# Optimization experiments

Measured on AMD Instinct MI355X. Metric: run time of the kernel, lower is better.

The kernel has to match this reference:

```python
import jax, jax.numpy as jnp
import numpy as np

N = 100000      # total nodes in batched SEAL subgraphs
E = 1600000     # total edges
B = 512         # number of subgraphs (batch of graphs)
F = 128         # input feature dim (data.x + DRNL one-hot, pre-concatenated)
H = 128         # gnn_hidden_channels
L = 3           # num_hops == num GNN hidden layers
K = 100         # sort-pool k
D_TOT = H * L + 1              # 385, total_latent_dim
C1, C2, KW2 = 16, 32, 5        # conv1d channels / kernel
DENSE = ((K - 2) // 2 + 1 - KW2 + 1) * C2   # 1472
MLP_H = 128


def setup_inputs() -> dict:
    key = jax.random.key(0)
    ks = jax.random.split(key, 20)
    s = 0.05
    inp = {
        "x": jax.random.normal(ks[0], (N, F), jnp.float32),
        "edge_index": jax.random.randint(ks[1], (2, E), 0, N, dtype=jnp.int32).astype(jnp.int64),
        "batch": jnp.sort(jax.random.randint(ks[2], (N,), 0, B, dtype=jnp.int32)).astype(jnp.int64),
        "k": K,
        # GCN layer weights: F->H, H->H, H->H, H->1
        "Wg0": jax.random.normal(ks[3], (F, H), jnp.float32) * s, "bg0": jnp.zeros((H,), jnp.float32),
        "Wg1": jax.random.normal(ks[4], (H, H), jnp.float32) * s, "bg1": jnp.zeros((H,), jnp.float32),
        "Wg2": jax.random.normal(ks[5], (H, H), jnp.float32) * s, "bg2": jnp.zeros((H,), jnp.float32),
        "Wg3": jax.random.normal(ks[6], (H, 1), jnp.float32) * s, "bg3": jnp.zeros((1,), jnp.float32),
        # Conv1d(1, 16, kernel=D_TOT, stride=D_TOT): equivalent to per-node dense [16, D_TOT]
        "W1": jax.random.normal(ks[7], (C1, D_TOT), jnp.float32) * s, "b1": jnp.zeros((C1,), jnp.float32),
        # Conv1d(16, 32, 5, 1)
        "W2": jax.random.normal(ks[8], (C2, C1, KW2), jnp.float32) * s, "b2": jnp.zeros((C2,), jnp.float32),
        # MLP [dense, mlp_hidden, 1]
        "Wm1": jax.random.normal(ks[9], (DENSE, MLP_H), jnp.float32) * s, "bm1": jnp.zeros((MLP_H,), jnp.float32),
        "Wm2": jax.random.normal(ks[10], (MLP_H, 1), jnp.float32) * s, "bm2": jnp.zeros((1,), jnp.float32),
    }
    return inp


def reference(x, edge_index, batch, k,
              Wg0, bg0, Wg1, bg1, Wg2, bg2, Wg3, bg3,
              W1, b1, W2, b2, Wm1, bm1, Wm2, bm2):
    n = x.shape[0]
    src, dst = edge_index[0], edge_index[1]
    loop = jnp.arange(n)
    srcL = jnp.concatenate([src, loop])   # add self-loops (GCNConv default)
    dstL = jnp.concatenate([dst, loop])
    deg = jax.ops.segment_sum(jnp.ones(srcL.shape[0], x.dtype), dstL, num_segments=n)
    dinv = jnp.where(deg > 0, jax.lax.rsqrt(deg), 0.0)
    norm = (dinv[srcL] * dinv[dstL])[:, None]   # symmetric normalization

    def gcn(h, W, b):
        msg = (h @ W)[srcL] * norm                      # [E+N, out]
        return jax.ops.segment_sum(msg, dstL, num_segments=n) + b

    xs = []
    h = x
    for W, b in ((Wg0, bg0), (Wg1, bg1), (Wg2, bg2), (Wg3, bg3)):
        h = jnp.tanh(gcn(h, W, b))
        xs.append(h)
    feat = jnp.concatenate(xs, axis=-1)                 # [n, D_TOT]

    # --- SortAggregation(k): per-graph sort by last channel, descending ---
    counts = jax.ops.segment_sum(jnp.ones(n, jnp.int32), batch, num_segments=B)
    # tanh output in [-1,1], so batch*4 dominates; ascending sort => grouped by graph,
    # descending within each graph by last channel.
    sort_key = batch.astype(feat.dtype) * 4.0 - feat[:, -1]
    feat_s = feat[jnp.argsort(sort_key)]
    starts = jnp.cumsum(counts) - counts                # exclusive prefix sum
    idx = starts[:, None] + jnp.arange(k)[None, :]      # [B, k]
    valid = jnp.arange(k)[None, :] < counts[:, None]
    pooled = jnp.where(valid[:, :, None], feat_s[jnp.clip(idx, 0, n - 1)], 0.0)  # [B, k, D_TOT]

    # conv1: Conv1d(1, 16, kernel=D_TOT, stride=D_TOT) on [B,1,k*D_TOT]
    h1 = jax.nn.relu(jnp.einsum('bkd,od->bok', pooled, W1) + b1[None, :, None])  # [B,16,k]
    # maxpool1d(2,2)
    h1 = h1.reshape(h1.shape[0], h1.shape[1], -1, 2).max(axis=-1)                # [B,16,k//2]
    # conv2: Conv1d(16, 32, 5, 1)
    h2 = jax.lax.conv_general_dilated(h1, W2, window_strides=(1,), padding='VALID',
                                      dimension_numbers=('NCH', 'OIH', 'NCH'))
    h2 = jax.nn.relu(h2 + b2[None, :, None])                                     # [B,32,k//2-4]
    flat = h2.reshape(h2.shape[0], -1)                                           # [B, DENSE]
    # MLP (dropout inactive at inference)
    hid = jax.nn.relu(flat @ Wm1 + bm1)
    return hid @ Wm2 + bm2                                                       # [B, 1]
```

## Files before the change

kernel.cpp:

```cpp
#include <hip/hip_runtime.h>
#include <hip/hip_bf16.h>
#include <cfloat>

#define F_IN   128
#define H_DIM  128
#define D_TOT  385
#define KTOP   100
#define C1     16
#define C2     32
#define KW2    5
#define POOLW  (KTOP/2)
#define CONV2W (POOLW - KW2 + 1)
#define DENSE  (C2*CONV2W)
#define MLPH   128
#define SORT_CAP 2048
#define D_PAD  388
#define C1SLOTS 32
#define SCHUNK 1024
#define AGG_NPB 8

__global__ void hist_kernel(const int* __restrict__ keys, int n, int nbins, int* __restrict__ cnt) {
    int i = blockIdx.x * blockDim.x + threadIdx.x;
    if (i < n) {
        int k = keys[i];
        k = (k < 0) ? 0 : (k >= nbins ? nbins - 1 : k);
        atomicAdd(&cnt[k], 1);
    }
}

__global__ void scan_excl_kernel(const int* __restrict__ cnt, int n,
                                 int* __restrict__ start, int* __restrict__ cursor,
                                 float* __restrict__ dinv) {
    __shared__ int s[1024];
    __shared__ int carry_s;
    int tid = threadIdx.x;
    if (tid == 0) carry_s = 0;
    __syncthreads();
    for (int base = 0; base < n; base += 1024) {
        int i = base + tid;
        int v = (i < n) ? cnt[i] : 0;
        s[tid] = v;
        __syncthreads();
        for (int off = 1; off < 1024; off <<= 1) {
            int t = (tid >= off) ? s[tid - off] : 0;
            __syncthreads();
            s[tid] += t;
            __syncthreads();
        }
        int excl = s[tid] - v;
        int carry = carry_s;
        if (i < n) {
            start[i] = carry + excl;
            if (cursor) cursor[i] = carry + excl;
            if (dinv)   dinv[i]   = rsqrtf((float)v + 1.0f);
        }
        __syncthreads();
        if (tid == 0) carry_s += s[1023];
        __syncthreads();
    }
}

__global__ __launch_bounds__(256) void chunksum_kernel(const int* __restrict__ cnt, int n,
                                                       int* __restrict__ bsum) {
    __shared__ int red[256];
    int blk = blockIdx.x, tid = threadIdx.x;
    int base = blk * SCHUNK;
    int s = 0;
    for (int idx = tid; idx < SCHUNK; idx += 256) {
        int i = base + idx;
        s += (i < n) ? cnt[i] : 0;
    }
    red[tid] = s; __syncthreads();
    for (int off = 128; off > 0; off >>= 1) {
        if (tid < off) red[tid] += red[tid + off];
        __syncthreads();
    }
    if (tid == 0) bsum[blk] = red[0];
}

__global__ __launch_bounds__(256) void scan_apply_kernel(const int* __restrict__ cnt, int n,
                                                         const int* __restrict__ bstart,
                                                         int* __restrict__ start,
                                                         int* __restrict__ cursor,
                                                         float* __restrict__ dinv) {
    __shared__ int tsum[256];
    int blk = blockIdx.x, tid = threadIdx.x;
    int base = blk * SCHUNK + tid * 4;
    int v[4];
    #pragma unroll
    for (int k = 0; k < 4; k++) { int i = base + k; v[k] = (i < n) ? cnt[i] : 0; }
    int loc = v[0] + v[1] + v[2] + v[3];
    tsum[tid] = loc; __syncthreads();
    int x = loc;
    for (int off = 1; off < 256; off <<= 1) {
        int t = (tid >= off) ? tsum[tid - off] : 0;
        __syncthreads();
        x += t; tsum[tid] = x;
        __syncthreads();
    }
    int run = x - loc + bstart[blk];
    #pragma unroll
    for (int k = 0; k < 4; k++) {
        int i = base + k;
        if (i < n) {
            start[i]  = run;
            cursor[i] = run;
            dinv[i]   = rsqrtf((float)v[k] + 1.0f);
        }
        run += v[k];
    }
}

__global__ void csr_fill_kernel(const int* __restrict__ src, const int* __restrict__ dst, int e, int n,
                                int* __restrict__ cursor, const float* __restrict__ dinv,
                                int* __restrict__ csr_src, float* __restrict__ csr_w) {
    int i = blockIdx.x * blockDim.x + threadIdx.x;
    if (i < e) {
        int s = src[i], d = dst[i];
        s = (s < 0) ? 0 : (s >= n ? n - 1 : s);
        d = (d < 0) ? 0 : (d >= n ? n - 1 : d);
        int pos = atomicAdd(&cursor[d], 1);
        csr_src[pos] = s;
        csr_w[pos]   = dinv[s] * dinv[d];
    }
}

__global__ __launch_bounds__(256) void gemm_nk128(const float* __restrict__ A, int lda,
                                                  const float* __restrict__ W,
                                                  float* __restrict__ T, int n) {
    __shared__ float Al[64 * 128];
    __shared__ float Wl[128 * 64];
    int tid = threadIdx.x;
    int brow = blockIdx.x * 64;
    int chalf = blockIdx.y;

    for (int kk = tid >> 4; kk < 128; kk += 16) {
        int c4 = tid & 15;
        float4 w = *(const float4*)&W[kk * 128 + chalf * 64 + c4 * 4];
        *(float4*)&Wl[kk * 64 + c4 * 4] = w;
    }
    for (int idx = tid; idx < 64 * 128; idx += 256) {
        int rr = idx >> 7, k = idx & 127;
        int r = brow + rr;
        float a = (r < n) ? A[(size_t)r * lda + k] : 0.0f;
        Al[rr * 128 + (k ^ (rr & 31))] = a;
    }
    __syncthreads();

    int tr = tid >> 4, tc = tid & 15;
    int r0 = tr * 4;
    float acc[4][4] = {};
    #pragma unroll 4
    for (int k = 0; k < 128; k++) {
        float4 w = *(const float4*)&Wl[k * 64 + tc * 4];
        float a0 = Al[(r0 + 0) * 128 + (k ^ ((r0 + 0) & 31))];
        float a1 = Al[(r0 + 1) * 128 + (k ^ ((r0 + 1) & 31))];
        float a2 = Al[(r0 + 2) * 128 + (k ^ ((r0 + 2) & 31))];
        float a3 = Al[(r0 + 3) * 128 + (k ^ ((r0 + 3) & 31))];
        acc[0][0] += a0 * w.x; acc[0][1] += a0 * w.y; acc[0][2] += a0 * w.z; acc[0][3] += a0 * w.w;
        acc[1][0] += a1 * w.x; acc[1][1] += a1 * w.y; acc[1][2] += a1 * w.z; acc[1][3] += a1 * w.w;
        acc[2][0] += a2 * w.x; acc[2][1] += a2 * w.y; acc[2][2] += a2 * w.z; acc[2][3] += a2 * w.w;
        acc[3][0] += a3 * w.x; acc[3][1] += a3 * w.y; acc[3][2] += a3 * w.z; acc[3][3] += a3 * w.w;
    }
    for (int i = 0; i < 4; i++) {
        int r = brow + r0 + i;
        if (r < n) {
            float4 o = make_float4(acc[i][0], acc[i][1], acc[i][2], acc[i][3]);
            *(float4*)&T[(size_t)r * 128 + chalf * 64 + tc * 4] = o;
        }
    }
}

__global__ __launch_bounds__(256) void gcn_agg128(const float* __restrict__ T,
                                                  const int* __restrict__ csr_src,
                                                  const float* __restrict__ csr_w,
                                                  const int* __restrict__ row_start,
                                                  const int* __restrict__ cnt,
                                                  const float* __restrict__ dinv,
                                                  const float* __restrict__ bias,
                                                  float* __restrict__ feat, int layer, int n,
                                                  const float* __restrict__ Wg3,
                                                  float* __restrict__ T3) {
    int g    = threadIdx.x >> 5;
    int lane = threadIdx.x & 31;
    int i = blockIdx.x * AGG_NPB + g;
    if (i >= n) return;
    int c4 = lane << 2;
    float di = dinv[i];
    float s2 = di * di;
    float4 self = *(const float4*)&T[(size_t)i * 128 + c4];
    float4 acc = make_float4(self.x * s2, self.y * s2, self.z * s2, self.w * s2);
    int rs = row_start[i], ce = cnt[i];
    for (int e = 0; e < ce; e++) {
        int s  = csr_src[rs + e];
        float w = csr_w[rs + e];
        float4 v = *(const float4*)&T[(size_t)s * 128 + c4];
        acc.x += v.x * w; acc.y += v.y * w; acc.z += v.z * w; acc.w += v.w * w;
    }
    float4 bb = *(const float4*)&bias[c4];
    float4 vt = make_float4(tanhf(acc.x + bb.x), tanhf(acc.y + bb.y),
                            tanhf(acc.z + bb.z), tanhf(acc.w + bb.w));
    float* fout = &feat[(size_t)i * D_TOT + layer * 128 + c4];
    fout[0] = vt.x; fout[1] = vt.y; fout[2] = vt.z; fout[3] = vt.w;
    if (T3 != nullptr) {
        float4 wg = *(const float4*)&Wg3[c4];
        float4 p = make_float4(vt.x * wg.x, vt.y * wg.y, vt.z * wg.z, vt.w * wg.w);
        #pragma unroll
        for (int off = 16; off > 0; off >>= 1) {
            p.x += __shfl_down(p.x, off, 32);
            p.y += __shfl_down(p.y, off, 32);
            p.z += __shfl_down(p.z, off, 32);
            p.w += __shfl_down(p.w, off, 32);
        }
        if (lane == 0) T3[i] = (p.x + p.z) + (p.y + p.w);
    }
}

__global__ void gcn_agg1(const float* __restrict__ T3,
                         const int* __restrict__ csr_src, const float* __restrict__ csr_w,
                         const int* __restrict__ row_start, const int* __restrict__ cnt,
                         const float* __restrict__ dinv, const float* __restrict__ bg3,
                         float* __restrict__ feat, int n) {
    int i = blockIdx.x * blockDim.x + threadIdx.x;
    if (i >= n) return;
    float di = dinv[i];
    float acc = T3[i] * di * di;
    int rs = row_start[i], ce = cnt[i];
    for (int e = 0; e < ce; e++) acc += T3[csr_src[rs + e]] * csr_w[rs + e];
    feat[(size_t)i * D_TOT + (D_TOT - 1)] = tanhf(acc + bg3[0]);
}

__global__ __launch_bounds__(256) void sortpool_kernel(const float* __restrict__ feat,
                                                       const int* __restrict__ gcnt,
                                                       const int* __restrict__ gstart,
                                                       int* __restrict__ sel) {
    int b = blockIdx.x, tid = threadIdx.x;
    __shared__ float sv[SORT_CAP];
    __shared__ int   si[SORT_CAP];
    int cnt = gcnt[b];
    if (cnt > SORT_CAP) cnt = SORT_CAP;
    int start = gstart[b];
    if (cnt == 0) {
        for (int j = tid; j < KTOP; j += 256) sel[b * KTOP + j] = -1;
        return;
    }
    float bb = 4.0f * (float)b;
    int P = 1; while (P < cnt) P <<= 1;
    for (int j = tid; j < P; j += 256) {
        if (j < cnt) {
            float v = feat[(size_t)(start + j) * D_TOT + (D_TOT - 1)];
            sv[j] = bb - v;
            si[j] = j;
        } else { sv[j] = FLT_MAX; si[j] = j; }
    }
    __syncthreads();
    for (int ksz = 2; ksz <= P; ksz <<= 1) {
        for (int jj = ksz >> 1; jj > 0; jj >>= 1) {
            for (int t = tid; t < P; t += 256) {
                int l = t ^ jj;
                if (l > t) {
                    float va = sv[t], vb = sv[l];
                    int   ia = si[t], ib = si[l];
                    bool aFirst = (va < vb) || (va == vb && ia < ib);
                    bool up = ((t & ksz) == 0);
                    if (up ? !aFirst : aFirst) {
                        sv[t] = vb; sv[l] = va; si[t] = ib; si[l] = ia;
                    }
                }
            }
            __syncthreads();
        }
    }
    for (int j = tid; j < KTOP; j += 256)
        sel[b * KTOP + j] = (j < cnt) ? (start + si[j]) : -1;
}

__global__ __launch_bounds__(256) void conv1_kernel(const float* __restrict__ feat,
                                                    const int* __restrict__ sel,
                                                    const float* __restrict__ W1,
                                                    const float* __restrict__ b1,
                                                    float* __restrict__ h1, int nslots) {
    __shared__ float W1l[C1 * D_PAD];
    __shared__ float rows[C1SLOTS * D_PAD];
    int tid = threadIdx.x;
    int base = blockIdx.x * C1SLOTS;

    for (int idx = tid; idx < C1 * D_TOT; idx += 256) {
        int o = idx / D_TOT, t = idx - o * D_TOT;
        W1l[o * D_PAD + t] = W1[idx];
    }
    for (int idx = tid; idx < C1SLOTS * D_TOT; idx += 256) {
        int r = idx / D_TOT, t = idx - r * D_TOT;
        int slot = base + r;
        float v = 0.f;
        if (slot < nslots) {
            int row = sel[slot];
            if (row >= 0) v = feat[(size_t)row * D_TOT + t];
        }
        rows[r * D_PAD + t] = v;
    }
    __syncthreads();

    int g = tid >> 4, o = tid & 15;
    int r0 = 2 * g;
    const float* wr = &W1l[o * D_PAD];
    const float* p0 = &rows[r0 * D_PAD];
    const float* p1 = &rows[(r0 + 1) * D_PAD];
    float a0 = 0.f, a1 = 0.f;
    #pragma unroll 4
    for (int t = 0; t < 384; t += 4) {
        float4 w  = *(const float4*)&wr[t];
        float4 x0 = *(const float4*)&p0[t];
        float4 x1 = *(const float4*)&p1[t];
        a0 += x0.x * w.x + x0.y * w.y + x0.z * w.z + x0.w * w.w;
        a1 += x1.x * w.x + x1.y * w.y + x1.z * w.z + x1.w * w.w;
    }
    a0 += p0[384] * wr[384];
    a1 += p1[384] * wr[384];

    float bo = b1[o];
    int slot0 = base + r0;
    if (slot0 < nslots) {
        int b = slot0 / KTOP, j = slot0 - b * KTOP;
        h1[((size_t)b * C1 + o) * KTOP + j] = fmaxf(a0 + bo, 0.f);
    }
    int slot1 = slot0 + 1;
    if (slot1 < nslots) {
        int b = slot1 / KTOP, j = slot1 - b * KTOP;
        h1[((size_t)b * C1 + o) * KTOP + j] = fmaxf(a1 + bo, 0.f);
    }
}

__global__ __launch_bounds__(256) void head_kernel(const float* __restrict__ h1,
                                                   const float* __restrict__ W2, const float* __restrict__ b2,
                                                   const float* __restrict__ Wm1, const float* __restrict__ bm1,
                                                   const float* __restrict__ Wm2, const float* __restrict__ bm2,
                                                   float* __restrict__ out) {
    int b = blockIdx.x, tid = threadIdx.x;
    __shared__ float pool[C1 * POOLW];
    __shared__ float flat[DENSE];
    __shared__ float hid[MLPH];
    __shared__ float red[256];

    for (int p = tid; p < C1 * POOLW; p += 256) {
        int i = p / POOLW, t = p % POOLW;
        float v0 = h1[((size_t)b * C1 + i) * KTOP + 2 * t];
        float v1 = h1[((size_t)b * C1 + i) * KTOP + 2 * t + 1];
        pool[i * POOLW + t] = fmaxf(v0, v1);
    }
    __syncthreads();
    for (int q = tid; q < DENSE; q += 256) {
        int o = q / CONV2W, t = q % CONV2W;
        float acc = b2[o];
        #pragma unroll
        for (int i = 0; i < C1; i++) {
            #pragma unroll
            for (int ks = 0; ks < KW2; ks++)
                acc += pool[i * POOLW + t + ks] * W2[(o * C1 + i) * KW2 + ks];
        }
        flat[o * CONV2W + t] = fmaxf(acc, 0.f);
    }
    __syncthreads();
    {
        int h = tid & 127, part = tid >> 7;
        float acc = 0.f;
        for (int t = part * (DENSE / 2); t < (part + 1) * (DENSE / 2); t++)
            acc += flat[t] * Wm1[(size_t)t * MLPH + h];
        red[tid] = acc;
    }
    __syncthreads();
    if (tid < 128) hid[tid] = fmaxf(red[tid] + red[tid + 128] + bm1[tid], 0.f);
    __syncthreads();
    if (tid < 64) {
        float p = hid[tid] * Wm2[tid] + hid[tid + 64] * Wm2[tid + 64];
        #pragma unroll
        for (int off = 32; off > 0; off >>= 1) p += __shfl_down(p, off, 64);
        if (tid == 0) out[b] = p + bm2[0];
    }
}

extern "C" void kernel_launch(void* const* d_in, const int* in_sizes, int n_in,
                              void* d_out, int out_size, void* d_ws, size_t ws_size,
                              hipStream_t stream) {
    const float* x     = (const float*)d_in[0];
    const int*   ei    = (const int*)d_in[1];
    const int*   batch = (const int*)d_in[2];
    const float* Wg0 = (const float*)d_in[4],  *bg0 = (const float*)d_in[5];
    const float* Wg1 = (const float*)d_in[6],  *bg1 = (const float*)d_in[7];
    const float* Wg2 = (const float*)d_in[8],  *bg2 = (const float*)d_in[9];
    const float* Wg3 = (const float*)d_in[10], *bg3 = (const float*)d_in[11];
    const float* W1  = (const float*)d_in[12], *b1  = (const float*)d_in[13];
    const float* W2  = (const float*)d_in[14], *b2  = (const float*)d_in[15];
    const float* Wm1 = (const float*)d_in[16], *bm1 = (const float*)d_in[17];
    const float* Wm2 = (const float*)d_in[18], *bm2 = (const float*)d_in[19];
    float* out = (float*)d_out;

    const int N = in_sizes[2];
    const int E = in_sizes[1] / 2;
    const int B = out_size;
    const int* src = ei;
    const int* dst = ei + E;
    const int nb = (N + SCHUNK - 1) / SCHUNK;

    auto rup = [](size_t b) { return (b + 255) & ~(size_t)255; };
    size_t need = 0;
    need += rup((size_t)N * 4) * 4;
    need += rup((size_t)N * 4);
    need += rup((size_t)nb * 4) * 2;
    need += rup((size_t)B * 4) * 2;
    need += rup((size_t)E * 4) * 2;
    need += rup((size_t)N * 128 * 4);
    need += rup((size_t)N * D_TOT * 4);
    need += rup((size_t)B * KTOP * 4);
    need += rup((size_t)B * C1 * KTOP * 4);
    if (need > ws_size) {
        hipMemsetAsync(d_out, 0, (size_t)out_size * 4, stream);
        return;
    }

    char* p = (char*)d_ws;
    auto alloc = [&](size_t bytes) { void* r = (void*)p; p += (bytes + 255) & ~(size_t)255; return r; };
    int*   cnt_node  = (int*)alloc((size_t)N * 4);
    int*   row_start = (int*)alloc((size_t)N * 4);
    int*   cursor    = (int*)alloc((size_t)N * 4);
    float* dinv      = (float*)alloc((size_t)N * 4);
    float* T3        = (float*)alloc((size_t)N * 4);
    int*   bsum      = (int*)alloc((size_t)nb * 4);
    int*   bstart    = (int*)alloc((size_t)nb * 4);
    int*   gcnt      = (int*)alloc((size_t)B * 4);
    int*   gstart    = (int*)alloc((size_t)B * 4);
    int*   csr_src   = (int*)alloc((size_t)E * 4);
    float* csr_w     = (float*)alloc((size_t)E * 4);
    float* T         = (float*)alloc((size_t)N * 128 * 4);
    float* feat      = (float*)alloc((size_t)N * D_TOT * 4);
    int*   sel       = (int*)alloc((size_t)B * KTOP * 4);
    float* h1        = (float*)alloc((size_t)B * C1 * KTOP * 4);

    hipMemsetAsync(cnt_node, 0, (size_t)N * 4, stream);
    hipMemsetAsync(gcnt,     0, (size_t)B * 4, stream);

    hist_kernel<<<(E + 255) / 256, 256, 0, stream>>>(dst, E, N, cnt_node);
    hist_kernel<<<(N + 255) / 256, 256, 0, stream>>>(batch, N, B, gcnt);

    chunksum_kernel<<<nb, 256, 0, stream>>>(cnt_node, N, bsum);
    scan_excl_kernel<<<1, 1024, 0, stream>>>(bsum, nb, bstart, nullptr, nullptr);
    scan_apply_kernel<<<nb, 256, 0, stream>>>(cnt_node, N, bstart, row_start, cursor, dinv);
    scan_excl_kernel<<<1, 1024, 0, stream>>>(gcnt, B, gstart, nullptr, nullptr);

    csr_fill_kernel<<<(E + 255) / 256, 256, 0, stream>>>(src, dst, E, N, cursor, dinv, csr_src, csr_w);

    dim3 ggrid((N + 63) / 64, 2);
    const int agg_grid = (N + AGG_NPB - 1) / AGG_NPB;
    gemm_nk128<<<ggrid, 256, 0, stream>>>(x, F_IN, Wg0, T, N);
    gcn_agg128<<<agg_grid, 256, 0, stream>>>(T, csr_src, csr_w, row_start, cnt_node, dinv, bg0, feat, 0, N, nullptr, nullptr);
    gemm_nk128<<<ggrid, 256, 0, stream>>>(feat, D_TOT, Wg1, T, N);
    gcn_agg128<<<agg_grid, 256, 0, stream>>>(T, csr_src, csr_w, row_start, cnt_node, dinv, bg1, feat, 1, N, nullptr, nullptr);
    gemm_nk128<<<ggrid, 256, 0, stream>>>(feat + 128, D_TOT, Wg2, T, N);
    gcn_agg128<<<agg_grid, 256, 0, stream>>>(T, csr_src, csr_w, row_start, cnt_node, dinv, bg2, feat, 2, N, Wg3, T3);
    gcn_agg1<<<(N + 255) / 256, 256, 0, stream>>>(T3, csr_src, csr_w, row_start, cnt_node, dinv, bg3, feat, N);

    sortpool_kernel<<<B, 256, 0, stream>>>(feat, gcnt, gstart, sel);
    conv1_kernel<<<(B * KTOP + C1SLOTS - 1) / C1SLOTS, 256, 0, stream>>>(feat, sel, W1, b1, h1, B * KTOP);
    head_kernel<<<B, 256, 0, stream>>>(h1, W2, b2, Wm1, bm1, Wm2, bm2, out);
}
```

Baseline: 1.397 ms.

## Pad feature row stride to 388 and stream GEMM A operand from global

Feature matrix rows are padded from 385 to 388 floats so every row starts 16-byte aligned, which allows float4 stores in aggregation and float4 loads in the GEMM. The GEMM stops staging the A tile in shared memory. Each thread now reads its four rows directly from global memory as float4 while W stays in LDS. This removes the A-tile LDS traffic and the sync it needs, cuts LDS use for better occupancy, and lifts register-level reuse to four k steps per load. The cost is redundant global reads of A across the 16 column threads, which must be absorbed by the cache, and a slightly larger workspace.

```diff
diff --git a/kernel.cpp b/kernel.cpp
--- a/kernel.cpp
+++ b/kernel.cpp
@@ -5,6 +5,7 @@
 #define F_IN   128
 #define H_DIM  128
 #define D_TOT  385
+#define FSTR   388
 #define KTOP   100
 #define C1     16
 #define C2     32
@@ -128,7 +129,6 @@
 __global__ __launch_bounds__(256) void gemm_nk128(const float* __restrict__ A, int lda,
                                                   const float* __restrict__ W,
                                                   float* __restrict__ T, int n) {
-    __shared__ float Al[64 * 128];
     __shared__ float Wl[128 * 64];
     int tid = threadIdx.x;
     int brow = blockIdx.x * 64;
@@ -139,34 +139,44 @@
         float4 w = *(const float4*)&W[kk * 128 + chalf * 64 + c4 * 4];
         *(float4*)&Wl[kk * 64 + c4 * 4] = w;
     }
-    for (int idx = tid; idx < 64 * 128; idx += 256) {
-        int rr = idx >> 7, k = idx & 127;
-        int r = brow + rr;
-        float a = (r < n) ? A[(size_t)r * lda + k] : 0.0f;
-        Al[rr * 128 + (k ^ (rr & 31))] = a;
-    }
     __syncthreads();
 
     int tr = tid >> 4, tc = tid & 15;
-    int r0 = tr * 4;
+    int r0 = brow + tr * 4;
+    int c0 = tc * 4;
+    const float* pa0 = A + (size_t)((r0 + 0 < n) ? r0 + 0 : n - 1) * lda;
+    const float* pa1 = A + (size_t)((r0 + 1 < n) ? r0 + 1 : n - 1) * lda;
+    const float* pa2 = A + (size_t)((r0 + 2 < n) ? r0 + 2 : n - 1) * lda;
+    const float* pa3 = A + (size_t)((r0 + 3 < n) ? r0 + 3 : n - 1) * lda;
+
     float acc[4][4] = {};
-    #pragma unroll 4
-    for (int k = 0; k < 128; k++) {
-        float4 w = *(const float4*)&Wl[k * 64 + tc * 4];
-        float a0 = Al[(r0 + 0) * 128 + (k ^ ((r0 + 0) & 31))];
-        float a1 = Al[(r0 + 1) * 128 + (k ^ ((r0 + 1) & 31))];
-        float a2 = Al[(r0 + 2) * 128 + (k ^ ((r0 + 2) & 31))];
-        float a3 = Al[(r0 + 3) * 128 + (k ^ ((r0 + 3) & 31))];
-        acc[0][0] += a0 * w.x; acc[0][1] += a0 * w.y; acc[0][2] += a0 * w.z; acc[0][3] += a0 * w.w;
-        acc[1][0] += a1 * w.x; acc[1][1] += a1 * w.y; acc[1][2] += a1 * w.z; acc[1][3] += a1 * w.w;
-        acc[2][0] += a2 * w.x; acc[2][1] += a2 * w.y; acc[2][2] += a2 * w.z; acc[2][3] += a2 * w.w;
-        acc[3][0] += a3 * w.x; acc[3][1] += a3 * w.y; acc[3][2] += a3 * w.z; acc[3][3] += a3 * w.w;
+    #pragma unroll 8
+    for (int kk = 0; kk < 128; kk += 4) {
+        float4 a0 = *(const float4*)&pa0[kk];
+        float4 a1 = *(const float4*)&pa1[kk];
+        float4 a2 = *(const float4*)&pa2[kk];
+        float4 a3 = *(const float4*)&pa3[kk];
+        float4 w0 = *(const float4*)&Wl[(kk + 0) * 64 + c0];
+        float4 w1 = *(const float4*)&Wl[(kk + 1) * 64 + c0];
+        float4 w2 = *(const float4*)&Wl[(kk + 2) * 64 + c0];
+        float4 w3 = *(const float4*)&Wl[(kk + 3) * 64 + c0];
+        #define ROWFMA(i, ai)                                              \
+            acc[i][0] += ai.x * w0.x; acc[i][1] += ai.x * w0.y;            \
+            acc[i][2] += ai.x * w0.z; acc[i][3] += ai.x * w0.w;            \
+            acc[i][0] += ai.y * w1.x; acc[i][1] += ai.y * w1.y;            \
+            acc[i][2] += ai.y * w1.z; acc[i][3] += ai.y * w1.w;            \
+            acc[i][0] += ai.z * w2.x; acc[i][1] += ai.z * w2.y;            \
+            acc[i][2] += ai.z * w2.z; acc[i][3] += ai.z * w2.w;            \
+            acc[i][0] += ai.w * w3.x; acc[i][1] += ai.w * w3.y;            \
+            acc[i][2] += ai.w * w3.z; acc[i][3] += ai.w * w3.w;
+        ROWFMA(0, a0) ROWFMA(1, a1) ROWFMA(2, a2) ROWFMA(3, a3)
+        #undef ROWFMA
     }
     for (int i = 0; i < 4; i++) {
-        int r = brow + r0 + i;
+        int r = brow + tr * 4 + i;
         if (r < n) {
             float4 o = make_float4(acc[i][0], acc[i][1], acc[i][2], acc[i][3]);
-            *(float4*)&T[(size_t)r * 128 + chalf * 64 + tc * 4] = o;
+            *(float4*)&T[(size_t)r * 128 + chalf * 64 + c0] = o;
         }
     }
 }
@@ -200,8 +210,7 @@
     float4 bb = *(const float4*)&bias[c4];
     float4 vt = make_float4(tanhf(acc.x + bb.x), tanhf(acc.y + bb.y),
                             tanhf(acc.z + bb.z), tanhf(acc.w + bb.w));
-    float* fout = &feat[(size_t)i * D_TOT + layer * 128 + c4];
-    fout[0] = vt.x; fout[1] = vt.y; fout[2] = vt.z; fout[3] = vt.w;
+    *(float4*)&feat[(size_t)i * FSTR + layer * 128 + c4] = vt;
     if (T3 != nullptr) {
         float4 wg = *(const float4*)&Wg3[c4];
         float4 p = make_float4(vt.x * wg.x, vt.y * wg.y, vt.z * wg.z, vt.w * wg.w);
@@ -227,7 +236,7 @@
     float acc = T3[i] * di * di;
     int rs = row_start[i], ce = cnt[i];
     for (int e = 0; e < ce; e++) acc += T3[csr_src[rs + e]] * csr_w[rs + e];
-    feat[(size_t)i * D_TOT + (D_TOT - 1)] = tanhf(acc + bg3[0]);
+    feat[(size_t)i * FSTR + (D_TOT - 1)] = tanhf(acc + bg3[0]);
 }
 
 __global__ __launch_bounds__(256) void sortpool_kernel(const float* __restrict__ feat,
@@ -248,7 +257,7 @@
     int P = 1; while (P < cnt) P <<= 1;
     for (int j = tid; j < P; j += 256) {
         if (j < cnt) {
-            float v = feat[(size_t)(start + j) * D_TOT + (D_TOT - 1)];
+            float v = feat[(size_t)(start + j) * FSTR + (D_TOT - 1)];
             sv[j] = bb - v;
             si[j] = j;
         } else { sv[j] = FLT_MAX; si[j] = j; }
@@ -295,7 +304,7 @@
         float v = 0.f;
         if (slot < nslots) {
             int row = sel[slot];
-            if (row >= 0) v = feat[(size_t)row * D_TOT + t];
+            if (row >= 0) v = feat[(size_t)row * FSTR + t];
         }
         rows[r * D_PAD + t] = v;
     }
@@ -410,7 +419,7 @@
     need += rup((size_t)B * 4) * 2;
     need += rup((size_t)E * 4) * 2;
     need += rup((size_t)N * 128 * 4);
-    need += rup((size_t)N * D_TOT * 4);
+    need += rup((size_t)N * FSTR * 4);
     need += rup((size_t)B * KTOP * 4);
     need += rup((size_t)B * C1 * KTOP * 4);
     if (need > ws_size) {
@@ -432,7 +441,7 @@
     int*   csr_src   = (int*)alloc((size_t)E * 4);
     float* csr_w     = (float*)alloc((size_t)E * 4);
     float* T         = (float*)alloc((size_t)N * 128 * 4);
-    float* feat      = (float*)alloc((size_t)N * D_TOT * 4);
+    float* feat      = (float*)alloc((size_t)N * FSTR * 4);
     int*   sel       = (int*)alloc((size_t)B * KTOP * 4);
     float* h1        = (float*)alloc((size_t)B * C1 * KTOP * 4);
 
@@ -453,9 +462,9 @@
     const int agg_grid = (N + AGG_NPB - 1) / AGG_NPB;
     gemm_nk128<<<ggrid, 256, 0, stream>>>(x, F_IN, Wg0, T, N);
     gcn_agg128<<<agg_grid, 256, 0, stream>>>(T, csr_src, csr_w, row_start, cnt_node, dinv, bg0, feat, 0, N, nullptr, nullptr);
-    gemm_nk128<<<ggrid, 256, 0, stream>>>(feat, D_TOT, Wg1, T, N);
+    gemm_nk128<<<ggrid, 256, 0, stream>>>(feat, FSTR, Wg1, T, N);
     gcn_agg128<<<agg_grid, 256, 0, stream>>>(T, csr_src, csr_w, row_start, cnt_node, dinv, bg1, feat, 1, N, nullptr, nullptr);
-    gemm_nk128<<<ggrid, 256, 0, stream>>>(feat + 128, D_TOT, Wg2, T, N);
+    gemm_nk128<<<ggrid, 256, 0, stream>>>(feat + 128, FSTR, Wg2, T, N);
     gcn_agg128<<<agg_grid, 256, 0, stream>>>(T, csr_src, csr_w, row_start, cnt_node, dinv, bg2, feat, 2, N, Wg3, T3);
     gcn_agg1<<<(N + 255) / 256, 256, 0, stream>>>(T3, csr_src, csr_w, row_start, cnt_node, dinv, bg3, feat, N);
 
```

Result: faster. 1.189 ms (-14.9%).
